# Performance work log

Measured on AMD Instinct MI355X. Metric: run time of the kernel, lower is better.

## Reference

```python
import jax, jax.numpy as jnp
import numpy as np
from jax import lax

DIM = 256
MOTION = 128
HEADS = 8
HID = int(DIM * 3.0)
EPS = 1e-5


def std_ln(x, w, b):
    # standard nn.LayerNorm: biased var, /sqrt(var+eps)
    mean = x.mean(-1, keepdims=True)
    var = jnp.var(x, axis=-1, keepdims=True)
    return w * (x - mean) / jnp.sqrt(var + EPS) + b


def custom_ln(x, w, b):
    # repo's custom LayerNorm: UNBIASED std (ddof=1) and divide by (std+eps)
    mean = x.mean(-1, keepdims=True)
    std = jnp.std(x, axis=-1, ddof=1, keepdims=True)
    return w * (x - mean) / (std + EPS) + b


def setup_inputs() -> dict:
    key = jax.random.key(0)
    ks = jax.random.split(key, 32)
    s = 0.02
    d = {}
    d['x'] = jax.random.normal(ks[0], (4, 16384, DIM), jnp.float32)
    d['cor'] = jax.random.uniform(ks[1], (4, 128, 128, 2), jnp.float32)
    # attention projections (qkv_bias=False)
    d['q_w'] = jax.random.normal(ks[2], (DIM, DIM), jnp.float32) * s
    d['kv_w'] = jax.random.normal(ks[3], (2 * DIM, DIM), jnp.float32) * s
    d['cor_w'] = jax.random.normal(ks[4], (MOTION, 2), jnp.float32) * s
    hd = DIM // HEADS
    md = MOTION // HEADS
    d['kln_w'] = jnp.ones((HEADS, 1, hd), jnp.float32)
    d['kln_b'] = jnp.zeros((HEADS, 1, hd), jnp.float32)
    d['vln_w'] = jnp.ones((HEADS, 1, hd), jnp.float32)
    d['vln_b'] = jnp.zeros((HEADS, 1, hd), jnp.float32)
    d['corln_w'] = jnp.ones((HEADS, 1, md), jnp.float32)
    d['corln_b'] = jnp.zeros((HEADS, 1, md), jnp.float32)
    d['op1_w'] = jax.random.normal(ks[5], (DIM, DIM), jnp.float32) * s
    d['op1_b'] = jnp.zeros((DIM,), jnp.float32)
    d['op2_w'] = jax.random.normal(ks[6], (DIM, DIM), jnp.float32) * s
    d['op2_b'] = jnp.zeros((DIM,), jnp.float32)
    d['om1_w'] = jax.random.normal(ks[7], (MOTION, MOTION), jnp.float32) * s
    d['om1_b'] = jnp.zeros((MOTION,), jnp.float32)
    d['om2_w'] = jax.random.normal(ks[8], (MOTION, MOTION), jnp.float32) * s
    d['om2_b'] = jnp.zeros((MOTION,), jnp.float32)
    d['norm1_w'] = jnp.ones((DIM,), jnp.float32)
    d['norm1_b'] = jnp.zeros((DIM,), jnp.float32)
    d['norm2_w'] = jnp.ones((DIM,), jnp.float32)
    d['norm2_b'] = jnp.zeros((DIM,), jnp.float32)
    d['fc1_w'] = jax.random.normal(ks[9], (HID, DIM), jnp.float32) * s
    d['fc1_b'] = jnp.zeros((HID,), jnp.float32)
    d['dw_w'] = jax.random.normal(ks[10], (HID, 1, 3, 3), jnp.float32) * np.sqrt(2.0 / 9.0)
    d['dw_b'] = jnp.zeros((HID,), jnp.float32)
    d['fc2_w'] = jax.random.normal(ks[11], (DIM, HID), jnp.float32) * s
    d['fc2_b'] = jnp.zeros((DIM,), jnp.float32)
    d['H'] = 128
    d['W'] = 128
    d['B'] = 2
    return d


def _forward(x, cor, q_w, kv_w, cor_w, kln_w, kln_b, vln_w, vln_b,
             corln_w, corln_b, op1_w, op1_b, op2_w, op2_b,
             om1_w, om1_b, om2_w, om2_b, norm1_w, norm1_b,
             norm2_w, norm2_b, fc1_w, fc1_b, dw_w, dw_b, fc2_w, fc2_b,
             H, W, B):
    gelu = lambda t: jax.nn.gelu(t, approximate=False)
    nwB = 2 * B
    N = H * W
    C = x.shape[-1]
    M = cor_w.shape[0]
    h = kln_w.shape[0]
    hd = C // h
    md = M // h
    hid = fc1_w.shape[0]

    xw = x.reshape(nwB, N, C)            # window_partition with full window == identity
    corw = cor.reshape(nwB, N, 2)

    xn = std_ln(xw, norm1_w, norm1_b)
    half = nwB // 2
    xr = jnp.concatenate([xn[half:], xn[:half]], axis=0)  # swap frame halves

    q = (xn @ q_w.T).reshape(nwB, N, h, hd).transpose(0, 2, 1, 3)          # bhnd
    kv = (xr @ kv_w.T).reshape(nwB, N, 2, h, hd)
    k = kv[:, :, 0].transpose(0, 2, 1, 3)
    v = kv[:, :, 1].transpose(0, 2, 1, 3)
    ce_flat = corw @ cor_w.T                                               # (nwB,N,M)
    ce = ce_flat.reshape(nwB, N, h, md).transpose(0, 2, 1, 3)

    k = custom_ln(k, kln_w, kln_b)
    v = custom_ln(v, vln_w, vln_b)
    ce = custom_ln(ce, corln_w, corln_b)

    # linear attention: (k^T v)/N then q @ .
    ktv = jnp.einsum('bhnd,bhne->bhde', k, v) / N
    app = jnp.einsum('bhnd,bhde->bhne', q, ktv).transpose(0, 2, 1, 3).reshape(nwB, N, C)
    t = app + xn                                   # shortcut bias = x_norm
    x_app = gelu(t @ op1_w.T + op1_b) @ op2_w.T + op2_b + xn

    ktc = jnp.einsum('bhnd,bhne->bhde', k, ce) / N
    crev = jnp.einsum('bhnd,bhde->bhne', q, ktc).transpose(0, 2, 1, 3).reshape(nwB, N, M)
    dm = crev - ce_flat
    motion = gelu(dm @ om1_w.T + om1_b) @ om2_w.T + om2_b

    x_back = xn + x_app

    # Mlp with depthwise conv
    y = std_ln(x_back, norm2_w, norm2_b)
    h1 = y @ fc1_w.T + fc1_b                       # (nwB,N,hid)
    img = h1.transpose(0, 2, 1).reshape(nwB, hid, H, W)
    conv = lax.conv_general_dilated(img, dw_w, (1, 1), 'SAME',
                                    feature_group_count=hid,
                                    dimension_numbers=('NCHW', 'OIHW', 'NCHW'))
    conv = conv + dw_b[None, :, None, None]
    h2 = gelu(conv.reshape(nwB, hid, N).transpose(0, 2, 1))
    out = h2 @ fc2_w.T + fc2_b

    x_out = xw + out
    return x_out, motion


def reference(x, cor, q_w, kv_w, cor_w, kln_w, kln_b, vln_w, vln_b,
              corln_w, corln_b, op1_w, op1_b, op2_w, op2_b,
              om1_w, om1_b, om2_w, om2_b, norm1_w, norm1_b,
              norm2_w, norm2_b, fc1_w, fc1_b, dw_w, dw_b, fc2_w, fc2_b,
              H, W, B):
    return _forward(x, cor, q_w, kv_w, cor_w, kln_w, kln_b, vln_w, vln_b,
                    corln_w, corln_b, op1_w, op1_b, op2_w, op2_b,
                    om1_w, om1_b, om2_w, om2_b, norm1_w, norm1_b,
                    norm2_w, norm2_b, fc1_w, fc1_b, dw_w, dw_b, fc2_w, fc2_b,
                    H, W, B)
```

## Files before the change

kernel.cpp:

```cpp
#include <hip/hip_runtime.h>
#include <hip/hip_bf16.h>

#define NTOK 65536

typedef __attribute__((ext_vector_type(4))) float f32x4;
typedef __attribute__((ext_vector_type(8))) short bf16x8;

__device__ __forceinline__ float gelu_f(float x){
    float z = -2.30234438f * fmaf(0.044715f * x * x, x, x);
    float e = exp2f(z);
    return x * __builtin_amdgcn_rcpf(1.0f + e);
}
__device__ __forceinline__ float bf2f(unsigned short u){
    union { unsigned int i; float f; } w; w.i = ((unsigned int)u) << 16; return w.f;
}
__device__ __forceinline__ unsigned short f2bf(float f){
    __hip_bfloat16 h = __float2bfloat16(f);
    return *reinterpret_cast<unsigned short*>(&h);
}

__global__ __launch_bounds__(256) void wconv_kernel(const float* __restrict__ q_w, const float* __restrict__ kv_w,
                                                    const float* __restrict__ op1_w, const float* __restrict__ op2_w,
                                                    const float* __restrict__ om1_w, const float* __restrict__ om2_w,
                                                    const float* __restrict__ fc1_w, const float* __restrict__ fc2_w,
                                                    unsigned short* __restrict__ Wb){
    size_t e = ((size_t)blockIdx.x * 256 + threadIdx.x) * 4;
    if (e >= 753664) return;
    const float* src; size_t off;
    if      (e <  65536){ src = q_w;   off = 0; }
    else if (e < 196608){ src = kv_w;  off = 65536; }
    else if (e < 262144){ src = op1_w; off = 196608; }
    else if (e < 327680){ src = op2_w; off = 262144; }
    else if (e < 344064){ src = om1_w; off = 327680; }
    else if (e < 360448){ src = om2_w; off = 344064; }
    else if (e < 557056){ src = fc1_w; off = 360448; }
    else                { src = fc2_w; off = 557056; }
    float4 v = *reinterpret_cast<const float4*>(src + (e - off));
    ushort4 o; o.x = f2bf(v.x); o.y = f2bf(v.y); o.z = f2bf(v.z); o.w = f2bf(v.w);
    *reinterpret_cast<ushort4*>(Wb + e) = o;
}

template<bool BF16IN>
__global__ __launch_bounds__(256) void stdln_kernel(const void* __restrict__ Xp,
                                                    const float* __restrict__ w,
                                                    const float* __restrict__ b,
                                                    unsigned short* __restrict__ out){
    int wv = threadIdx.x >> 6, lane = threadIdx.x & 63;
    int tok0 = (blockIdx.x * 4 + wv) * 8;
    int c0 = lane * 4;
    float4 w4 = *reinterpret_cast<const float4*>(w + c0);
    float4 b4 = *reinterpret_cast<const float4*>(b + c0);
    #pragma unroll 2
    for (int j = 0; j < 8; j++){
        size_t base = (size_t)(tok0 + j) * 256 + c0;
        float v[4];
        if constexpr (BF16IN){
            ushort4 u = *reinterpret_cast<const ushort4*>((const unsigned short*)Xp + base);
            v[0] = bf2f(u.x); v[1] = bf2f(u.y); v[2] = bf2f(u.z); v[3] = bf2f(u.w);
        } else {
            float4 f = *reinterpret_cast<const float4*>((const float*)Xp + base);
            v[0] = f.x; v[1] = f.y; v[2] = f.z; v[3] = f.w;
        }
        float s = v[0] + v[1] + v[2] + v[3];
        #pragma unroll
        for (int m = 1; m < 64; m <<= 1) s += __shfl_xor(s, m, 64);
        float mean = s * (1.0f / 256.0f);
        float ss = 0;
        #pragma unroll
        for (int k = 0; k < 4; k++){ v[k] -= mean; ss = fmaf(v[k], v[k], ss); }
        #pragma unroll
        for (int m = 1; m < 64; m <<= 1) ss += __shfl_xor(ss, m, 64);
        float inv = rsqrtf(ss * (1.0f / 256.0f) + 1e-5f);
        ushort4 o;
        o.x = f2bf(w4.x * v[0] * inv + b4.x);
        o.y = f2bf(w4.y * v[1] * inv + b4.y);
        o.z = f2bf(w4.z * v[2] * inv + b4.z);
        o.w = f2bf(w4.w * v[3] * inv + b4.w);
        *reinterpret_cast<ushort4*>(out + base) = o;
    }
}

__global__ __launch_bounds__(256) void ce_kernel(const float* __restrict__ cor,
                                                 const float* __restrict__ cor_w,
                                                 unsigned short* __restrict__ CEF){
    int m = threadIdx.x & 127, half = threadIdx.x >> 7;
    float w0 = cor_w[m * 2 + 0], w1 = cor_w[m * 2 + 1];
    #pragma unroll 4
    for (int it = 0; it < 16; it++){
        int tok = blockIdx.x * 32 + it * 2 + half;
        float c0 = cor[(size_t)tok * 2 + 0];
        float c1 = cor[(size_t)tok * 2 + 1];
        CEF[(size_t)tok * 128 + m] = f2bf(c0 * w0 + c1 * w1);
    }
}

__global__ __launch_bounds__(256) void ktvc_kernel(const unsigned short* __restrict__ Kb,
                                                   const unsigned short* __restrict__ Vb,
                                                   const unsigned short* __restrict__ CEF,
                                                   const float* __restrict__ kw, const float* __restrict__ kbb,
                                                   const float* __restrict__ vw, const float* __restrict__ vbb,
                                                   const float* __restrict__ cw, const float* __restrict__ cbb,
                                                   float* __restrict__ KTV, float* __restrict__ KTC){
    int bh = blockIdx.x, b = bh >> 3, h = bh & 7;
    __shared__ float Ks[64][33];
    __shared__ float Vs[64][33];
    __shared__ float Cs[64][17];
    int t = threadIdx.x;
    int lr = t >> 2, lq = t & 3;
    int d0 = (t >> 4) * 2, e0 = (t & 15) * 2, e1 = t & 15;
    float kwr[8], kbr[8], vwr[8], vbr[8], cwr[4], cbr[4];
    #pragma unroll
    for (int j = 0; j < 8; j++){
        kwr[j] = kw[h * 32 + lq * 8 + j]; kbr[j] = kbb[h * 32 + lq * 8 + j];
        vwr[j] = vw[h * 32 + lq * 8 + j]; vbr[j] = vbb[h * 32 + lq * 8 + j];
    }
    #pragma unroll
    for (int j = 0; j < 4; j++){
        cwr[j] = cw[h * 16 + lq * 4 + j]; cbr[j] = cbb[h * 16 + lq * 4 + j];
    }
    float a00 = 0, a01 = 0, a10 = 0, a11 = 0;
    float c0a = 0, c1a = 0;
    size_t base = ((size_t)b << 14) + (size_t)blockIdx.y * 1024;
    for (int n0 = 0; n0 < 1024; n0 += 64){
        size_t rowi = base + n0 + lr;
        const ushort4* kp = reinterpret_cast<const ushort4*>(Kb + rowi * 256 + h * 32 + lq * 8);
        ushort4 ka = kp[0], kc = kp[1];
        const ushort4* vp = reinterpret_cast<const ushort4*>(Vb + rowi * 256 + h * 32 + lq * 8);
        ushort4 va = vp[0], vc = vp[1];
        ushort4 ca = *reinterpret_cast<const ushort4*>(CEF + rowi * 128 + h * 16 + lq * 4);
        float kvv[8] = { bf2f(ka.x), bf2f(ka.y), bf2f(ka.z), bf2f(ka.w),
                         bf2f(kc.x), bf2f(kc.y), bf2f(kc.z), bf2f(kc.w) };
        float vvv[8] = { bf2f(va.x), bf2f(va.y), bf2f(va.z), bf2f(va.w),
                         bf2f(vc.x), bf2f(vc.y), bf2f(vc.z), bf2f(vc.w) };
        float cvv[4] = { bf2f(ca.x), bf2f(ca.y), bf2f(ca.z), bf2f(ca.w) };
        float s = 0;
        #pragma unroll
        for (int j = 0; j < 8; j++) s += kvv[j];
        s += __shfl_xor(s, 1, 64); s += __shfl_xor(s, 2, 64);
        float mean = s * (1.0f / 32.0f);
        float ss = 0;
        #pragma unroll
        for (int j = 0; j < 8; j++){ kvv[j] -= mean; ss = fmaf(kvv[j], kvv[j], ss); }
        ss += __shfl_xor(ss, 1, 64); ss += __shfl_xor(ss, 2, 64);
        float inv = 1.0f / (sqrtf(ss * (1.0f / 31.0f)) + 1e-5f);
        #pragma unroll
        for (int j = 0; j < 8; j++) kvv[j] = fmaf(kwr[j] * kvv[j], inv, kbr[j]);
        s = 0;
        #pragma unroll
        for (int j = 0; j < 8; j++) s += vvv[j];
        s += __shfl_xor(s, 1, 64); s += __shfl_xor(s, 2, 64);
        mean = s * (1.0f / 32.0f);
        ss = 0;
        #pragma unroll
        for (int j = 0; j < 8; j++){ vvv[j] -= mean; ss = fmaf(vvv[j], vvv[j], ss); }
        ss += __shfl_xor(ss, 1, 64); ss += __shfl_xor(ss, 2, 64);
        inv = 1.0f / (sqrtf(ss * (1.0f / 31.0f)) + 1e-5f);
        #pragma unroll
        for (int j = 0; j < 8; j++) vvv[j] = fmaf(vwr[j] * vvv[j], inv, vbr[j]);
        s = 0;
        #pragma unroll
        for (int j = 0; j < 4; j++) s += cvv[j];
        s += __shfl_xor(s, 1, 64); s += __shfl_xor(s, 2, 64);
        mean = s * (1.0f / 16.0f);
        ss = 0;
        #pragma unroll
        for (int j = 0; j < 4; j++){ cvv[j] -= mean; ss = fmaf(cvv[j], cvv[j], ss); }
        ss += __shfl_xor(ss, 1, 64); ss += __shfl_xor(ss, 2, 64);
        inv = 1.0f / (sqrtf(ss * (1.0f / 15.0f)) + 1e-5f);
        #pragma unroll
        for (int j = 0; j < 4; j++) cvv[j] = fmaf(cwr[j] * cvv[j], inv, cbr[j]);
        __syncthreads();
        #pragma unroll
        for (int j = 0; j < 8; j++){ Ks[lr][lq * 8 + j] = kvv[j]; Vs[lr][lq * 8 + j] = vvv[j]; }
        #pragma unroll
        for (int j = 0; j < 4; j++) Cs[lr][lq * 4 + j] = cvv[j];
        __syncthreads();
        #pragma unroll 4
        for (int n = 0; n < 64; n++){
            float k0 = Ks[n][d0], k1 = Ks[n][d0 + 1];
            float v0 = Vs[n][e0], v1 = Vs[n][e0 + 1];
            float ce = Cs[n][e1];
            a00 = fmaf(k0, v0, a00); a01 = fmaf(k0, v1, a01);
            a10 = fmaf(k1, v0, a10); a11 = fmaf(k1, v1, a11);
            c0a = fmaf(k0, ce, c0a); c1a = fmaf(k1, ce, c1a);
        }
    }
    const float sc = 1.0f / 16384.0f;
    float* o = KTV + (size_t)bh * 1024;
    atomicAdd(&o[(d0 + 0) * 32 + e0 + 0], a00 * sc);
    atomicAdd(&o[(d0 + 0) * 32 + e0 + 1], a01 * sc);
    atomicAdd(&o[(d0 + 1) * 32 + e0 + 0], a10 * sc);
    atomicAdd(&o[(d0 + 1) * 32 + e0 + 1], a11 * sc);
    float* o2 = KTC + (size_t)bh * 512;
    atomicAdd(&o2[(d0 + 0) * 16 + e1], c0a * sc);
    atomicAdd(&o2[(d0 + 1) * 16 + e1], c1a * sc);
}

__global__ __launch_bounds__(256) void wcomb_kernel(const float* __restrict__ q_w,
                                                    const float* __restrict__ KTV,
                                                    const float* __restrict__ KTC,
                                                    unsigned short* __restrict__ WTC){
    int c = blockIdx.x;
    int b = blockIdx.y;
    int i = threadIdx.x;
    __shared__ float coef[32];
    int h = (c < 256) ? (c >> 5) : ((c - 256) >> 4);
    if (i < 32){
        if (c < 256) coef[i] = KTV[(size_t)((b * 8 + h) << 10) + i * 32 + (c & 31)];
        else         coef[i] = KTC[(size_t)((b * 8 + h) << 9)  + i * 16 + ((c - 256) & 15)];
    }
    __syncthreads();
    float acc = 0;
    #pragma unroll
    for (int d = 0; d < 32; d++) acc = fmaf(q_w[(size_t)(h * 32 + d) * 256 + i], coef[d], acc);
    WTC[((size_t)b * 384 + c) * 256 + i] = f2bf(acc);
}

__global__ __launch_bounds__(384) void dwconv_kernel(const unsigned short* __restrict__ H1,
                                                     const float* __restrict__ dww,
                                                     const float* __restrict__ dwb,
                                                     unsigned short* __restrict__ H2){
    int blk = blockIdx.x;
    int sub = threadIdx.x >= 192;
    int tid = threadIdx.x - (sub ? 192 : 0);
    int bb = blk >> 8;
    int yy = (blk >> 1) & 127;
    int xq = ((blk & 1) << 1) | sub;
    int x0 = xq * 32;
    int ch = tid * 4;
    float w[9][4];
    #pragma unroll
    for (int k = 0; k < 9; k++)
        #pragma unroll
        for (int j = 0; j < 4; j++) w[k][j] = dww[(ch + j) * 9 + k];
    float bias[4] = { dwb[ch], dwb[ch+1], dwb[ch+2], dwb[ch+3] };
    const bool r0v = (yy > 0), r2v = (yy < 127);
    size_t rowbase0 = ((size_t)((bb << 14) + ((yy - 1) << 7))) * 768 + ch;
    size_t rowbase1 = ((size_t)((bb << 14) + ( yy      << 7))) * 768 + ch;
    size_t rowbase2 = ((size_t)((bb << 14) + ((yy + 1) << 7))) * 768 + ch;
    size_t obase = ((size_t)((bb << 14) + (yy << 7))) * 768 + ch;

    ushort4 rA[3], rB[3], rC[3], rD[3];
    #define LOADR(DST, XX) do {                                               \
        int _x = (XX);                                                        \
        bool xv = ((unsigned)_x <= 127u);                                     \
        DST[0] = (xv && r0v) ? *reinterpret_cast<const ushort4*>(H1 + rowbase0 + (size_t)_x * 768) : ushort4{0,0,0,0}; \
        DST[1] = (xv)        ? *reinterpret_cast<const ushort4*>(H1 + rowbase1 + (size_t)_x * 768) : ushort4{0,0,0,0}; \
        DST[2] = (xv && r2v) ? *reinterpret_cast<const ushort4*>(H1 + rowbase2 + (size_t)_x * 768) : ushort4{0,0,0,0}; \
    } while (0)

    #define EMITX(SA, SB, SC, XX) do {                                        \
        float acc[4];                                                         \
        _Pragma("unroll")                                                     \
        for (int j = 0; j < 4; j++) acc[j] = bias[j];                         \
        _Pragma("unroll")                                                     \
        for (int r = 0; r < 3; r++){                                          \
            float a0=bf2f(SA[r].x),a1=bf2f(SA[r].y),a2=bf2f(SA[r].z),a3=bf2f(SA[r].w); \
            float b0=bf2f(SB[r].x),b1=bf2f(SB[r].y),b2=bf2f(SB[r].z),b3=bf2f(SB[r].w); \
            float c0=bf2f(SC[r].x),c1=bf2f(SC[r].y),c2=bf2f(SC[r].z),c3=bf2f(SC[r].w); \
            acc[0]=fmaf(a0,w[r*3+0][0],acc[0]); acc[0]=fmaf(b0,w[r*3+1][0],acc[0]); acc[0]=fmaf(c0,w[r*3+2][0],acc[0]); \
            acc[1]=fmaf(a1,w[r*3+0][1],acc[1]); acc[1]=fmaf(b1,w[r*3+1][1],acc[1]); acc[1]=fmaf(c1,w[r*3+2][1],acc[1]); \
            acc[2]=fmaf(a2,w[r*3+0][2],acc[2]); acc[2]=fmaf(b2,w[r*3+1][2],acc[2]); acc[2]=fmaf(c2,w[r*3+2][2],acc[2]); \
            acc[3]=fmaf(a3,w[r*3+0][3],acc[3]); acc[3]=fmaf(b3,w[r*3+1][3],acc[3]); acc[3]=fmaf(c3,w[r*3+2][3],acc[3]); \
        }                                                                     \
        ushort4 o;                                                            \
        o.x = f2bf(gelu_f(acc[0])); o.y = f2bf(gelu_f(acc[1]));               \
        o.z = f2bf(gelu_f(acc[2])); o.w = f2bf(gelu_f(acc[3]));               \
        *reinterpret_cast<ushort4*>(H2 + obase + (size_t)(XX) * 768) = o;     \
    } while (0)

    LOADR(rD, x0 - 1);
    LOADR(rA, x0);
    LOADR(rB, x0 + 1);
    LOADR(rC, x0 + 2);
    #pragma unroll 1
    for (int g = 0; g < 8; g++){
        int x = x0 + g * 4;
        EMITX(rD, rA, rB, x);     LOADR(rD, x + 3);
        EMITX(rA, rB, rC, x + 1); LOADR(rA, x + 4);
        EMITX(rB, rC, rD, x + 2); LOADR(rB, x + 5);
        EMITX(rC, rD, rA, x + 3); LOADR(rC, x + 6);
    }
    #undef LOADR
    #undef EMITX
}

#define M_KV        1
#define M_BIAS_GELU 2
#define M_BIAS_ADD2 3
#define M_BIAS      4
#define M_BIAS_BF16 5
#define M_BIAS_ADDX 6
#define M_ATTN      7

template<int MODE, bool SWAP, int K, int O>
__global__ __launch_bounds__(256) void mgemm(const unsigned short* __restrict__ A,
                                             const unsigned short* __restrict__ Wp,
                                             const float* __restrict__ bias,
                                             const void* __restrict__ add,
                                             void* __restrict__ out0,
                                             void* __restrict__ out1){
    __shared__ __align__(16) unsigned short As[2][128 * 32];
    __shared__ __align__(16) unsigned short Bs[2][128 * 32];
    const int t = threadIdx.x;
    const int lane = t & 63, wid = t >> 6;
    const int wm = wid >> 1, wn = wid & 1;
    const int row0 = blockIdx.x * 128;
    const int col0 = blockIdx.y * 128;
    const unsigned short* W = Wp;
    if constexpr (MODE == M_ATTN) W += (size_t)(row0 >> 14) * (384 * 256);
    f32x4 acc[4][4];
    #pragma unroll
    for (int i = 0; i < 4; i++)
        #pragma unroll
        for (int j = 0; j < 4; j++){ f32x4 z = {0.f, 0.f, 0.f, 0.f}; acc[i][j] = z; }

    const int lr = lane >> 2;
    const int ls = lane & 3;
    const int kq = lane >> 4;
    const int rr = lane & 15;

    auto STAGE = [&](int buf, int kb){
        #pragma unroll
        for (int i = 0; i < 2; i++){
            int r = i * 64 + wid * 16 + lr;
            int ko = ls ^ ((r >> 1) & 3);
            int ga = row0 + r;
            if (SWAP) ga ^= 32768;
            __builtin_amdgcn_global_load_lds(
                (const __attribute__((address_space(1))) unsigned int*)(A + (size_t)ga * K + kb + ko * 8),
                (__attribute__((address_space(3))) unsigned int*)(As[buf] + (i * 64 + wid * 16) * 32),
                16, 0, 0);
            __builtin_amdgcn_global_load_lds(
                (const __attribute__((address_space(1))) unsigned int*)(W + (size_t)(col0 + r) * K + kb + ko * 8),
                (__attribute__((address_space(3))) unsigned int*)(Bs[buf] + (i * 64 + wid * 16) * 32),
                16, 0, 0);
        }
    };

    constexpr int NT = K / 32;
    STAGE(0, 0);
    asm volatile("s_waitcnt vmcnt(0)" ::: "memory");
    __builtin_amdgcn_s_barrier();
    #pragma unroll 1
    for (int tt = 0; tt < NT; tt++){
        int cur = tt & 1;
        if (tt + 1 < NT) STAGE(cur ^ 1, (tt + 1) * 32);
        bf16x8 af[4], bfr[4];
        #pragma unroll
        for (int m = 0; m < 4; m++){
            int row = wm * 64 + m * 16 + rr;
            int s = kq ^ ((row >> 1) & 3);
            af[m] = *reinterpret_cast<const bf16x8*>(As[cur] + row * 32 + s * 8);
        }
        #pragma unroll
        for (int n = 0; n < 4; n++){
            int row = wn * 64 + n * 16 + rr;
            int s = kq ^ ((row >> 1) & 3);
            bfr[n] = *reinterpret_cast<const bf16x8*>(Bs[cur] + row * 32 + s * 8);
        }
        #pragma unroll
        for (int m = 0; m < 4; m++)
            #pragma unroll
            for (int n = 0; n < 4; n++)
                acc[m][n] = __builtin_amdgcn_mfma_f32_16x16x32_bf16(af[m], bfr[n], acc[m][n], 0, 0, 0);
        if (tt + 1 < NT){
            asm volatile("s_waitcnt vmcnt(0)" ::: "memory");
            __builtin_amdgcn_s_barrier();
        }
    }

    #pragma unroll
    for (int m = 0; m < 4; m++){
        #pragma unroll
        for (int n = 0; n < 4; n++){
            int col = col0 + wn * 64 + n * 16 + rr;
            int rbase = row0 + wm * 64 + m * 16 + kq * 4;
            #pragma unroll
            for (int j = 0; j < 4; j++){
                int r = rbase + j;
                float v = acc[m][n][j];
                size_t o = (size_t)r * O + col;
                if constexpr (MODE == M_KV){
                    if (col < 256) ((unsigned short*)out0)[(size_t)r * 256 + col] = f2bf(v);
                    else           ((unsigned short*)out1)[(size_t)r * 256 + col - 256] = f2bf(v);
                } else if constexpr (MODE == M_BIAS_GELU){
                    ((unsigned short*)out0)[o] = f2bf(gelu_f(v + bias[col]));
                } else if constexpr (MODE == M_BIAS_ADD2){
                    ((unsigned short*)out0)[o] = f2bf(v + bias[col] + 2.0f * bf2f(((const unsigned short*)add)[o]));
                } else if constexpr (MODE == M_BIAS){
                    ((float*)out0)[o] = v + bias[col];
                } else if constexpr (MODE == M_BIAS_BF16){
                    ((unsigned short*)out0)[o] = f2bf(v + bias[col]);
                } else if constexpr (MODE == M_BIAS_ADDX){
                    ((float*)out0)[o] = v + bias[col] + ((const float*)add)[o];
                } else if constexpr (MODE == M_ATTN){
                    if (col < 256){
                        size_t o1 = (size_t)r * 256 + col;
                        ((unsigned short*)out0)[o1] = f2bf(v + bf2f(((const unsigned short*)add)[o1]));
                    } else {
                        size_t o2 = (size_t)r * 128 + (col - 256);
                        ((unsigned short*)out1)[o2] = f2bf(v - bf2f(((const unsigned short*)bias)[o2]));
                    }
                }
            }
        }
    }
}

extern "C" void kernel_launch(void* const* d_in, const int* in_sizes, int n_in,
                              void* d_out, int out_size, void* d_ws, size_t ws_size,
                              hipStream_t stream){
    const float* x     = (const float*)d_in[0];
    const float* cor   = (const float*)d_in[1];
    const float* q_w   = (const float*)d_in[2];
    const float* kv_w  = (const float*)d_in[3];
    const float* cor_w = (const float*)d_in[4];
    const float* kln_w = (const float*)d_in[5];
    const float* kln_b = (const float*)d_in[6];
    const float* vln_w = (const float*)d_in[7];
    const float* vln_b = (const float*)d_in[8];
    const float* corln_w = (const float*)d_in[9];
    const float* corln_b = (const float*)d_in[10];
    const float* op1_w = (const float*)d_in[11];
    const float* op1_b = (const float*)d_in[12];
    const float* op2_w = (const float*)d_in[13];
    const float* op2_b = (const float*)d_in[14];
    const float* om1_w = (const float*)d_in[15];
    const float* om1_b = (const float*)d_in[16];
    const float* om2_w = (const float*)d_in[17];
    const float* om2_b = (const float*)d_in[18];
    const float* n1_w  = (const float*)d_in[19];
    const float* n1_b  = (const float*)d_in[20];
    const float* n2_w  = (const float*)d_in[21];
    const float* n2_b  = (const float*)d_in[22];
    const float* fc1_w = (const float*)d_in[23];
    const float* fc1_b = (const float*)d_in[24];
    const float* dw_w  = (const float*)d_in[25];
    const float* dw_b  = (const float*)d_in[26];
    const float* fc2_w = (const float*)d_in[27];
    const float* fc2_b = (const float*)d_in[28];

    unsigned short* XN  = (unsigned short*)d_ws;
    unsigned short* Qb  = XN  + (size_t)NTOK * 256;
    unsigned short* Kb  = Qb  + (size_t)NTOK * 256;
    unsigned short* Vb  = Kb  + (size_t)NTOK * 256;
    unsigned short* CEF = Vb  + (size_t)NTOK * 256;
    unsigned short* CE  = CEF + (size_t)NTOK * 128;
    float* KTV = (float*)(CE + (size_t)NTOK * 128);
    float* KTC = KTV + 32768;
    unsigned short* WTC = (unsigned short*)(KTC + 16384);
    unsigned short* Wb  = WTC + 4 * 384 * 256;
    unsigned short* H2  = Wb + 753664;
    unsigned short* T1 = Vb;
    unsigned short* T2 = Kb;
    unsigned short* XB = Qb;
    unsigned short* Y  = Vb;
    unsigned short* TM = CE;
    unsigned short* MH = CEF;
    unsigned short* H1 = XN;
    float* xout = (float*)d_out;
    float* mout = xout + (size_t)NTOK * 256;

    unsigned short* w_kv  = Wb + 65536;
    unsigned short* w_op1 = Wb + 196608;
    unsigned short* w_op2 = Wb + 262144;
    unsigned short* w_om1 = Wb + 327680;
    unsigned short* w_om2 = Wb + 344064;
    unsigned short* w_fc1 = Wb + 360448;
    unsigned short* w_fc2 = Wb + 557056;

    wconv_kernel<<<736, 256, 0, stream>>>(q_w, kv_w, op1_w, op2_w, om1_w, om2_w, fc1_w, fc2_w, Wb);
    stdln_kernel<false><<<2048, 256, 0, stream>>>(x, n1_w, n1_b, XN);
    mgemm<M_KV, true, 256, 512><<<dim3(512, 4), 256, 0, stream>>>(XN, w_kv, nullptr, nullptr, Kb, Vb);
    ce_kernel<<<2048, 256, 0, stream>>>(cor, cor_w, CEF);
    hipMemsetAsync(KTV, 0, (32768 + 16384) * sizeof(float), stream);
    ktvc_kernel<<<dim3(32, 16), 256, 0, stream>>>(Kb, Vb, CEF, kln_w, kln_b, vln_w, vln_b,
                                                  corln_w, corln_b, KTV, KTC);
    wcomb_kernel<<<dim3(384, 4), 256, 0, stream>>>(q_w, KTV, KTC, WTC);
    mgemm<M_ATTN, false, 256, 384><<<dim3(512, 3), 256, 0, stream>>>(XN, WTC, (const float*)CEF, XN, T1, TM);
    mgemm<M_BIAS_GELU, false, 256, 256><<<dim3(512, 2), 256, 0, stream>>>(T1, w_op1, op1_b, nullptr, T2, nullptr);
    mgemm<M_BIAS_ADD2, false, 256, 256><<<dim3(512, 2), 256, 0, stream>>>(T2, w_op2, op2_b, XN, XB, nullptr);
    mgemm<M_BIAS_GELU, false, 128, 128><<<dim3(512, 1), 256, 0, stream>>>(TM, w_om1, om1_b, nullptr, MH, nullptr);
    mgemm<M_BIAS, false, 128, 128><<<dim3(512, 1), 256, 0, stream>>>(MH, w_om2, om2_b, nullptr, mout, nullptr);
    stdln_kernel<true><<<2048, 256, 0, stream>>>(XB, n2_w, n2_b, Y);
    mgemm<M_BIAS_BF16, false, 256, 768><<<dim3(512, 6), 256, 0, stream>>>(Y, w_fc1, fc1_b, nullptr, H1, nullptr);
    dwconv_kernel<<<1024, 384, 0, stream>>>(H1, dw_w, dw_b, H2);
    mgemm<M_BIAS_ADDX, false, 768, 256><<<dim3(512, 2), 256, 0, stream>>>(H2, w_fc2, fc2_b, x, xout, nullptr);
}
```

Before: 495.0 us.

## Widen GEMM N-tiles to reuse A across columns; block dwconv over rows

The GEMM kernel is templated on the number of column waves, so one block now covers up to 384 output columns with up to 768 threads. Each A tile is then staged once per block instead of once per column block, which removes the repeated A reads. The depthwise conv now computes 4 output rows per thread and keeps 6 input rows in registers, so vertical halo rows are loaded less often. In exchange the grid has fewer, larger blocks, LDS use rises for the wide B tiles, and the conv carries more registers per thread, which may lower occupancy.

```diff
diff --git a/kernel.cpp b/kernel.cpp
--- a/kernel.cpp
+++ b/kernel.cpp
@@ -216,73 +216,82 @@
     WTC[((size_t)b * 384 + c) * 256 + i] = f2bf(acc);
 }
 
-__global__ __launch_bounds__(384) void dwconv_kernel(const unsigned short* __restrict__ H1,
+__global__ __launch_bounds__(192) void dwconv_kernel(const unsigned short* __restrict__ H1,
                                                      const float* __restrict__ dww,
                                                      const float* __restrict__ dwb,
                                                      unsigned short* __restrict__ H2){
     int blk = blockIdx.x;
-    int sub = threadIdx.x >= 192;
-    int tid = threadIdx.x - (sub ? 192 : 0);
-    int bb = blk >> 8;
-    int yy = (blk >> 1) & 127;
-    int xq = ((blk & 1) << 1) | sub;
-    int x0 = xq * 32;
-    int ch = tid * 4;
+    int xq = blk & 3;
+    int yb = (blk >> 2) & 31;
+    int bb = blk >> 7;
+    int y0 = yb * 4, x0 = xq * 32;
+    int ch = threadIdx.x * 4;
     float w[9][4];
     #pragma unroll
     for (int k = 0; k < 9; k++)
         #pragma unroll
         for (int j = 0; j < 4; j++) w[k][j] = dww[(ch + j) * 9 + k];
     float bias[4] = { dwb[ch], dwb[ch+1], dwb[ch+2], dwb[ch+3] };
-    const bool r0v = (yy > 0), r2v = (yy < 127);
-    size_t rowbase0 = ((size_t)((bb << 14) + ((yy - 1) << 7))) * 768 + ch;
-    size_t rowbase1 = ((size_t)((bb << 14) + ( yy      << 7))) * 768 + ch;
-    size_t rowbase2 = ((size_t)((bb << 14) + ((yy + 1) << 7))) * 768 + ch;
-    size_t obase = ((size_t)((bb << 14) + (yy << 7))) * 768 + ch;
-
-    ushort4 rA[3], rB[3], rC[3], rD[3];
+    size_t rb[6]; bool rv[6];
+    #pragma unroll
+    for (int r = 0; r < 6; r++){
+        int yr = y0 - 1 + r;
+        rv[r] = ((unsigned)yr <= 127u);
+        int yc = yr < 0 ? 0 : (yr > 127 ? 127 : yr);
+        rb[r] = ((size_t)((bb << 14) + (yc << 7))) * 768 + ch;
+    }
+    size_t ob[4];
+    #pragma unroll
+    for (int j = 0; j < 4; j++) ob[j] = ((size_t)((bb << 14) + ((y0 + j) << 7))) * 768 + ch;
+
+    ushort4 cA[6], cB[6], cC[6], cD[6];
+    const ushort4 Z = {0, 0, 0, 0};
     #define LOADR(DST, XX) do {                                               \
         int _x = (XX);                                                        \
         bool xv = ((unsigned)_x <= 127u);                                     \
-        DST[0] = (xv && r0v) ? *reinterpret_cast<const ushort4*>(H1 + rowbase0 + (size_t)_x * 768) : ushort4{0,0,0,0}; \
-        DST[1] = (xv)        ? *reinterpret_cast<const ushort4*>(H1 + rowbase1 + (size_t)_x * 768) : ushort4{0,0,0,0}; \
-        DST[2] = (xv && r2v) ? *reinterpret_cast<const ushort4*>(H1 + rowbase2 + (size_t)_x * 768) : ushort4{0,0,0,0}; \
+        _Pragma("unroll")                                                     \
+        for (int r = 0; r < 6; r++)                                           \
+            DST[r] = (xv && rv[r]) ? *reinterpret_cast<const ushort4*>(H1 + rb[r] + (size_t)_x * 768) : Z; \
     } while (0)
 
-    #define EMITX(SA, SB, SC, XX) do {                                        \
-        float acc[4];                                                         \
+    #define EMITB(SA, SB, SC, XX) do {                                        \
         _Pragma("unroll")                                                     \
-        for (int j = 0; j < 4; j++) acc[j] = bias[j];                         \
-        _Pragma("unroll")                                                     \
-        for (int r = 0; r < 3; r++){                                          \
-            float a0=bf2f(SA[r].x),a1=bf2f(SA[r].y),a2=bf2f(SA[r].z),a3=bf2f(SA[r].w); \
-            float b0=bf2f(SB[r].x),b1=bf2f(SB[r].y),b2=bf2f(SB[r].z),b3=bf2f(SB[r].w); \
-            float c0=bf2f(SC[r].x),c1=bf2f(SC[r].y),c2=bf2f(SC[r].z),c3=bf2f(SC[r].w); \
-            acc[0]=fmaf(a0,w[r*3+0][0],acc[0]); acc[0]=fmaf(b0,w[r*3+1][0],acc[0]); acc[0]=fmaf(c0,w[r*3+2][0],acc[0]); \
-            acc[1]=fmaf(a1,w[r*3+0][1],acc[1]); acc[1]=fmaf(b1,w[r*3+1][1],acc[1]); acc[1]=fmaf(c1,w[r*3+2][1],acc[1]); \
-            acc[2]=fmaf(a2,w[r*3+0][2],acc[2]); acc[2]=fmaf(b2,w[r*3+1][2],acc[2]); acc[2]=fmaf(c2,w[r*3+2][2],acc[2]); \
-            acc[3]=fmaf(a3,w[r*3+0][3],acc[3]); acc[3]=fmaf(b3,w[r*3+1][3],acc[3]); acc[3]=fmaf(c3,w[r*3+2][3],acc[3]); \
+        for (int j = 0; j < 4; j++){                                          \
+            float acc[4];                                                     \
+            _Pragma("unroll")                                                 \
+            for (int q = 0; q < 4; q++) acc[q] = bias[q];                     \
+            _Pragma("unroll")                                                 \
+            for (int rr2 = 0; rr2 < 3; rr2++){                                \
+                int ri = j + rr2;                                             \
+                float a0=bf2f(SA[ri].x),a1=bf2f(SA[ri].y),a2=bf2f(SA[ri].z),a3=bf2f(SA[ri].w); \
+                float b0=bf2f(SB[ri].x),b1=bf2f(SB[ri].y),b2=bf2f(SB[ri].z),b3=bf2f(SB[ri].w); \
+                float c0=bf2f(SC[ri].x),c1=bf2f(SC[ri].y),c2=bf2f(SC[ri].z),c3=bf2f(SC[ri].w); \
+                acc[0]=fmaf(a0,w[rr2*3+0][0],acc[0]); acc[0]=fmaf(b0,w[rr2*3+1][0],acc[0]); acc[0]=fmaf(c0,w[rr2*3+2][0],acc[0]); \
+                acc[1]=fmaf(a1,w[rr2*3+0][1],acc[1]); acc[1]=fmaf(b1,w[rr2*3+1][1],acc[1]); acc[1]=fmaf(c1,w[rr2*3+2][1],acc[1]); \
+                acc[2]=fmaf(a2,w[rr2*3+0][2],acc[2]); acc[2]=fmaf(b2,w[rr2*3+1][2],acc[2]); acc[2]=fmaf(c2,w[rr2*3+2][2],acc[2]); \
+                acc[3]=fmaf(a3,w[rr2*3+0][3],acc[3]); acc[3]=fmaf(b3,w[rr2*3+1][3],acc[3]); acc[3]=fmaf(c3,w[rr2*3+2][3],acc[3]); \
+            }                                                                 \
+            ushort4 o;                                                        \
+            o.x = f2bf(gelu_f(acc[0])); o.y = f2bf(gelu_f(acc[1]));           \
+            o.z = f2bf(gelu_f(acc[2])); o.w = f2bf(gelu_f(acc[3]));           \
+            *reinterpret_cast<ushort4*>(H2 + ob[j] + (size_t)(XX) * 768) = o; \
         }                                                                     \
-        ushort4 o;                                                            \
-        o.x = f2bf(gelu_f(acc[0])); o.y = f2bf(gelu_f(acc[1]));               \
-        o.z = f2bf(gelu_f(acc[2])); o.w = f2bf(gelu_f(acc[3]));               \
-        *reinterpret_cast<ushort4*>(H2 + obase + (size_t)(XX) * 768) = o;     \
     } while (0)
 
-    LOADR(rD, x0 - 1);
-    LOADR(rA, x0);
-    LOADR(rB, x0 + 1);
-    LOADR(rC, x0 + 2);
+    LOADR(cD, x0 - 1);
+    LOADR(cA, x0);
+    LOADR(cB, x0 + 1);
+    LOADR(cC, x0 + 2);
     #pragma unroll 1
     for (int g = 0; g < 8; g++){
         int x = x0 + g * 4;
-        EMITX(rD, rA, rB, x);     LOADR(rD, x + 3);
-        EMITX(rA, rB, rC, x + 1); LOADR(rA, x + 4);
-        EMITX(rB, rC, rD, x + 2); LOADR(rB, x + 5);
-        EMITX(rC, rD, rA, x + 3); LOADR(rC, x + 6);
+        EMITB(cD, cA, cB, x);     LOADR(cD, x + 3);
+        EMITB(cA, cB, cC, x + 1); LOADR(cA, x + 4);
+        EMITB(cB, cC, cD, x + 2); LOADR(cB, x + 5);
+        EMITB(cC, cD, cA, x + 3); LOADR(cC, x + 6);
     }
     #undef LOADR
-    #undef EMITX
+    #undef EMITB
 }
 
 #define M_KV        1
@@ -293,20 +302,24 @@
 #define M_BIAS_ADDX 6
 #define M_ATTN      7
 
-template<int MODE, bool SWAP, int K, int O>
-__global__ __launch_bounds__(256) void mgemm(const unsigned short* __restrict__ A,
-                                             const unsigned short* __restrict__ Wp,
-                                             const float* __restrict__ bias,
-                                             const void* __restrict__ add,
-                                             void* __restrict__ out0,
-                                             void* __restrict__ out1){
+template<int MODE, bool SWAP, int K, int O, int WN>
+__global__ __launch_bounds__(128 * WN) void mgemm(const unsigned short* __restrict__ A,
+                                                  const unsigned short* __restrict__ Wp,
+                                                  const float* __restrict__ bias,
+                                                  const void* __restrict__ add,
+                                                  void* __restrict__ out0,
+                                                  void* __restrict__ out1){
+    constexpr int WAVES = 2 * WN;
+    constexpr int BN = 64 * WN;
+    constexpr int CH = 8 + 4 * WN;
+    constexpr int NT = K / 32;
     __shared__ __align__(16) unsigned short As[2][128 * 32];
-    __shared__ __align__(16) unsigned short Bs[2][128 * 32];
+    __shared__ __align__(16) unsigned short Bs[2][BN * 32];
     const int t = threadIdx.x;
     const int lane = t & 63, wid = t >> 6;
-    const int wm = wid >> 1, wn = wid & 1;
+    const int wm = wid & 1, wn = wid >> 1;
     const int row0 = blockIdx.x * 128;
-    const int col0 = blockIdx.y * 128;
+    const int colB = blockIdx.y * BN;
     const unsigned short* W = Wp;
     if constexpr (MODE == M_ATTN) W += (size_t)(row0 >> 14) * (384 * 256);
     f32x4 acc[4][4];
@@ -322,23 +335,27 @@
 
     auto STAGE = [&](int buf, int kb){
         #pragma unroll
-        for (int i = 0; i < 2; i++){
-            int r = i * 64 + wid * 16 + lr;
-            int ko = ls ^ ((r >> 1) & 3);
-            int ga = row0 + r;
-            if (SWAP) ga ^= 32768;
-            __builtin_amdgcn_global_load_lds(
-                (const __attribute__((address_space(1))) unsigned int*)(A + (size_t)ga * K + kb + ko * 8),
-                (__attribute__((address_space(3))) unsigned int*)(As[buf] + (i * 64 + wid * 16) * 32),
-                16, 0, 0);
-            __builtin_amdgcn_global_load_lds(
-                (const __attribute__((address_space(1))) unsigned int*)(W + (size_t)(col0 + r) * K + kb + ko * 8),
-                (__attribute__((address_space(3))) unsigned int*)(Bs[buf] + (i * 64 + wid * 16) * 32),
-                16, 0, 0);
+        for (int c = wid; c < CH; c += WAVES){
+            int r16 = (c < 8) ? c : (c - 8);
+            int row = r16 * 16 + lr;
+            int ko = ls ^ ((row >> 1) & 3);
+            if (c < 8){
+                int ga = row0 + row;
+                if (SWAP) ga ^= 32768;
+                __builtin_amdgcn_global_load_lds(
+                    (const __attribute__((address_space(1))) unsigned int*)(A + (size_t)ga * K + kb + ko * 8),
+                    (__attribute__((address_space(3))) unsigned int*)(As[buf] + r16 * 512),
+                    16, 0, 0);
+            } else {
+                int gc = colB + row;
+                __builtin_amdgcn_global_load_lds(
+                    (const __attribute__((address_space(1))) unsigned int*)(W + (size_t)gc * K + kb + ko * 8),
+                    (__attribute__((address_space(3))) unsigned int*)(Bs[buf] + r16 * 512),
+                    16, 0, 0);
+            }
         }
     };
 
-    constexpr int NT = K / 32;
     STAGE(0, 0);
     asm volatile("s_waitcnt vmcnt(0)" ::: "memory");
     __builtin_amdgcn_s_barrier();
@@ -374,7 +391,7 @@
     for (int m = 0; m < 4; m++){
         #pragma unroll
         for (int n = 0; n < 4; n++){
-            int col = col0 + wn * 64 + n * 16 + rr;
+            int col = colB + wn * 64 + n * 16 + rr;
             int rbase = row0 + wm * 64 + m * 16 + kq * 4;
             #pragma unroll
             for (int j = 0; j < 4; j++){
@@ -472,19 +489,19 @@
 
     wconv_kernel<<<736, 256, 0, stream>>>(q_w, kv_w, op1_w, op2_w, om1_w, om2_w, fc1_w, fc2_w, Wb);
     stdln_kernel<false><<<2048, 256, 0, stream>>>(x, n1_w, n1_b, XN);
-    mgemm<M_KV, true, 256, 512><<<dim3(512, 4), 256, 0, stream>>>(XN, w_kv, nullptr, nullptr, Kb, Vb);
+    mgemm<M_KV, true, 256, 512, 4><<<dim3(512, 2), 512, 0, stream>>>(XN, w_kv, nullptr, nullptr, Kb, Vb);
     ce_kernel<<<2048, 256, 0, stream>>>(cor, cor_w, CEF);
     hipMemsetAsync(KTV, 0, (32768 + 16384) * sizeof(float), stream);
     ktvc_kernel<<<dim3(32, 16), 256, 0, stream>>>(Kb, Vb, CEF, kln_w, kln_b, vln_w, vln_b,
                                                   corln_w, corln_b, KTV, KTC);
     wcomb_kernel<<<dim3(384, 4), 256, 0, stream>>>(q_w, KTV, KTC, WTC);
-    mgemm<M_ATTN, false, 256, 384><<<dim3(512, 3), 256, 0, stream>>>(XN, WTC, (const float*)CEF, XN, T1, TM);
-    mgemm<M_BIAS_GELU, false, 256, 256><<<dim3(512, 2), 256, 0, stream>>>(T1, w_op1, op1_b, nullptr, T2, nullptr);
-    mgemm<M_BIAS_ADD2, false, 256, 256><<<dim3(512, 2), 256, 0, stream>>>(T2, w_op2, op2_b, XN, XB, nullptr);
-    mgemm<M_BIAS_GELU, false, 128, 128><<<dim3(512, 1), 256, 0, stream>>>(TM, w_om1, om1_b, nullptr, MH, nullptr);
-    mgemm<M_BIAS, false, 128, 128><<<dim3(512, 1), 256, 0, stream>>>(MH, w_om2, om2_b, nullptr, mout, nullptr);
+    mgemm<M_ATTN, false, 256, 384, 6><<<dim3(512, 1), 768, 0, stream>>>(XN, WTC, (const float*)CEF, XN, T1, TM);
+    mgemm<M_BIAS_GELU, false, 256, 256, 4><<<dim3(512, 1), 512, 0, stream>>>(T1, w_op1, op1_b, nullptr, T2, nullptr);
+    mgemm<M_BIAS_ADD2, false, 256, 256, 4><<<dim3(512, 1), 512, 0, stream>>>(T2, w_op2, op2_b, XN, XB, nullptr);
+    mgemm<M_BIAS_GELU, false, 128, 128, 2><<<dim3(512, 1), 256, 0, stream>>>(TM, w_om1, om1_b, nullptr, MH, nullptr);
+    mgemm<M_BIAS, false, 128, 128, 2><<<dim3(512, 1), 256, 0, stream>>>(MH, w_om2, om2_b, nullptr, mout, nullptr);
     stdln_kernel<true><<<2048, 256, 0, stream>>>(XB, n2_w, n2_b, Y);
-    mgemm<M_BIAS_BF16, false, 256, 768><<<dim3(512, 6), 256, 0, stream>>>(Y, w_fc1, fc1_b, nullptr, H1, nullptr);
-    dwconv_kernel<<<1024, 384, 0, stream>>>(H1, dw_w, dw_b, H2);
-    mgemm<M_BIAS_ADDX, false, 768, 256><<<dim3(512, 2), 256, 0, stream>>>(H2, w_fc2, fc2_b, x, xout, nullptr);
-}
+    mgemm<M_BIAS_BF16, false, 256, 768, 6><<<dim3(512, 2), 768, 0, stream>>>(Y, w_fc1, fc1_b, nullptr, H1, nullptr);
+    dwconv_kernel<<<512, 192, 0, stream>>>(H1, dw_w, dw_b, H2);
+    mgemm<M_BIAS_ADDX, false, 768, 256, 4><<<dim3(512, 1), 512, 0, stream>>>(H2, w_fc2, fc2_b, x, xout, nullptr);
+}
```

Measured after the change: 443.8 us. -10.3%, faster.
